# Performance work log

Hardware: AMD Instinct MI355X
Metric: run time of the kernel (lower is better)

## Reference

```python
import jax, jax.numpy as jnp
import numpy as np

KERNEL = 7          # kernel_size
DIL = 1             # dilation
PAD = 3             # padding (same output size for k=7, d=1, s=1)
STRIDE = 1


def setup_inputs() -> dict:
    key = jax.random.key(0)
    x = jax.random.normal(key, (4, 256, 64, 64), dtype=jnp.float32)
    return {"x": x}


def reference(x):
    b, c, h, w = x.shape
    k2 = KERNEL * KERNEL
    # im2col / F.unfold equivalent: (b, c*k2, h_out, w_out), features ordered
    # (channel, kh, kw) exactly like torch.nn.functional.unfold.
    patches = jax.lax.conv_general_dilated_patches(
        x,
        filter_shape=(KERNEL, KERNEL),
        window_strides=(STRIDE, STRIDE),
        padding=[(PAD, PAD), (PAD, PAD)],
        rhs_dilation=(DIL, DIL),
    )
    ho, wo = patches.shape[2], patches.shape[3]
    p = patches.reshape(b, c, k2, ho, wo)          # (b, c, k2, h, w)
    center = p[:, :, k2 // 2]                      # (b, c, h, w) center of window
    # per-pixel similarity of each window element to the center, over channels
    sim = jnp.einsum('bckhw,bchw->bkhw', p, center)  # (b, k2, h, w)
    attn = jax.nn.softmax(sim, axis=1)               # softmax over window dim
    # weighted sum of window features
    out = jnp.einsum('bkhw,bckhw->bchw', attn, p)    # (b, c, h, w)
    return out
```

## Files before the change

### kernel.cpp

```cpp
#include <hip/hip_runtime.h>

typedef float f4 __attribute__((ext_vector_type(4)));

#define Hdim 64
#define Wdim 64
#define Cdim 256
#define HW (Hdim * Wdim)

__global__ __launch_bounds__(512, 4) void selfattn_kernel(const float* __restrict__ x,
                                                          float* __restrict__ out)
{
    const int bid = blockIdx.x;
    const int k   = bid & 7;
    const int seq = bid >> 3;
    const int b   = k >> 1;
    const int h   = (k & 1) * 32 + (seq >> 1);
    const int wbase = (seq & 1) * 32;
    const int t = threadIdx.x;

    __shared__ float simRed[49][32];
    __shared__ float attnBuf[49][32];
    __shared__ float redBuf[7][32];
    __shared__ float psumBuf[7][32];

    const float* xb = x + (size_t)b * (Cdim * HW);

    {
        const int w4 = t & 7;
        const int cp = (t >> 3) & 7;
        const int dy = t >> 6;
        const int lw0 = w4 * 4;
        const int w0g = wbase + lw0;

        if (dy < 7) {
            float sim[7][4];
            #pragma unroll
            for (int dx = 0; dx < 7; ++dx)
                #pragma unroll
                for (int p = 0; p < 4; ++p) sim[dx][p] = 0.f;

            const int row = h + dy - 3;
            if (row >= 0 && row < Hdim) {
                const bool hasL = (w0g != 0);
                const bool hasR = (w0g != 60);
                const float* xr = xb + (size_t)cp * HW + row * Wdim;
                const float* xc = xb + (size_t)cp * HW + h   * Wdim;
                for (int i = 0; i < 32; ++i) {
                    float f[12];
                    if (hasL) {
                        f4 v = *(const f4*)(xr + w0g - 4);
                        f[0]=v.x; f[1]=v.y; f[2]=v.z; f[3]=v.w;
                    } else { f[0]=0.f; f[1]=0.f; f[2]=0.f; f[3]=0.f; }
                    {
                        f4 v = *(const f4*)(xr + w0g);
                        f[4]=v.x; f[5]=v.y; f[6]=v.z; f[7]=v.w;
                    }
                    if (hasR) {
                        f4 v = *(const f4*)(xr + w0g + 4);
                        f[8]=v.x; f[9]=v.y; f[10]=v.z; f[11]=v.w;
                    } else { f[8]=0.f; f[9]=0.f; f[10]=0.f; f[11]=0.f; }
                    f4 cen = *(const f4*)(xc + w0g);
                    #pragma unroll
                    for (int dx = 0; dx < 7; ++dx)
                        #pragma unroll
                        for (int p = 0; p < 4; ++p)
                            sim[dx][p] += cen[p] * f[dx + p + 1];
                    xr += 8 * HW;
                    xc += 8 * HW;
                }
            }
            #pragma unroll
            for (int dx = 0; dx < 7; ++dx)
                #pragma unroll
                for (int p = 0; p < 4; ++p) {
                    float v = sim[dx][p];
                    v += __shfl_xor(v, 8);
                    v += __shfl_xor(v, 16);
                    v += __shfl_xor(v, 32);
                    sim[dx][p] = v;
                }
            if (cp == 0) {
                #pragma unroll
                for (int dx = 0; dx < 7; ++dx)
                    *(f4*)&simRed[dy * 7 + dx][lw0] = *(const f4*)sim[dx];
            }
        }
    }
    __syncthreads();

    {
        const int w  = t & 31;
        const int kc = t >> 5;
        float sred[7], e[7];
        if (kc < 7) {
            float lmax = -3.0e38f;
            #pragma unroll
            for (int jj = 0; jj < 7; ++jj) {
                float s = simRed[kc * 7 + jj][w];
                sred[jj] = s;
                lmax = fmaxf(lmax, s);
            }
            redBuf[kc][w] = lmax;
        }
        __syncthreads();
        if (kc < 7) {
            float m = redBuf[0][w];
            #pragma unroll
            for (int q = 1; q < 7; ++q) m = fmaxf(m, redBuf[q][w]);
            float ps = 0.f;
            #pragma unroll
            for (int jj = 0; jj < 7; ++jj) {
                e[jj] = __expf(sred[jj] - m);
                ps += e[jj];
            }
            psumBuf[kc][w] = ps;
        }
        __syncthreads();
        if (kc < 7) {
            float l = psumBuf[0][w];
            #pragma unroll
            for (int q = 1; q < 7; ++q) l += psumBuf[q][w];
            float rinv = 1.0f / l;
            #pragma unroll
            for (int jj = 0; jj < 7; ++jj)
                attnBuf[kc * 7 + jj][w] = e[jj] * rinv;
        }
    }
    __syncthreads();

    {
        const int w4 = t & 7;
        const int ci = t >> 3;
        const int lw0 = w4 * 4;
        const int w0g = wbase + lw0;
        const int c0 = ci * 4;
        const bool hasL = (w0g != 0);
        const bool hasR = (w0g != 60);

        float acc[4][4];
        #pragma unroll
        for (int ch = 0; ch < 4; ++ch)
            #pragma unroll
            for (int p = 0; p < 4; ++p) acc[ch][p] = 0.f;

        for (int dy = 0; dy < 7; ++dy) {
            const int row = h + dy - 3;
            if (row < 0 || row >= Hdim) continue;
            float a[7][4];
            #pragma unroll
            for (int dx = 0; dx < 7; ++dx) {
                f4 v = *(const f4*)&attnBuf[dy * 7 + dx][lw0];
                a[dx][0]=v.x; a[dx][1]=v.y; a[dx][2]=v.z; a[dx][3]=v.w;
            }
            const float* xr = xb + (size_t)c0 * HW + row * Wdim;
            #pragma unroll
            for (int ch = 0; ch < 4; ++ch) {
                float f[12];
                if (hasL) {
                    f4 v = *(const f4*)(xr + w0g - 4);
                    f[0]=v.x; f[1]=v.y; f[2]=v.z; f[3]=v.w;
                } else { f[0]=0.f; f[1]=0.f; f[2]=0.f; f[3]=0.f; }
                {
                    f4 v = *(const f4*)(xr + w0g);
                    f[4]=v.x; f[5]=v.y; f[6]=v.z; f[7]=v.w;
                }
                if (hasR) {
                    f4 v = *(const f4*)(xr + w0g + 4);
                    f[8]=v.x; f[9]=v.y; f[10]=v.z; f[11]=v.w;
                } else { f[8]=0.f; f[9]=0.f; f[10]=0.f; f[11]=0.f; }
                #pragma unroll
                for (int dx = 0; dx < 7; ++dx)
                    #pragma unroll
                    for (int p = 0; p < 4; ++p)
                        acc[ch][p] += a[dx][p] * f[dx + p + 1];
                xr += HW;
            }
        }

        float* ob = out + (size_t)b * (Cdim * HW) + h * Wdim + wbase;
        #pragma unroll
        for (int ch = 0; ch < 4; ++ch)
            *(f4*)(ob + (size_t)(c0 + ch) * HW + lw0) = *(const f4*)acc[ch];
    }
}

extern "C" void kernel_launch(void* const* d_in, const int* in_sizes, int n_in,
                              void* d_out, int out_size, void* d_ws, size_t ws_size,
                              hipStream_t stream)
{
    const float* x = (const float*)d_in[0];
    float* out = (float*)d_out;
    selfattn_kernel<<<dim3(512), 512, 0, stream>>>(x, out);
}
```

Baseline: 40.31 us.

## Split fused kernel into similarity and output kernels with channel-split grids

Replaces the single fused kernel with two kernels. The first computes partial window similarities over half the channels per block into a workspace. The second sums the two partials, applies the softmax, and computes the weighted output for half the channels per block. Each kernel runs 1024 blocks instead of 512, which raises parallelism and lets the first kernel drop idle threads. The cost is an extra launch, a workspace round trip, and softmax recomputed twice per pixel group. The fused kernel is kept as a fallback when the workspace is too small.

```diff
diff --git a/kernel.cpp b/kernel.cpp
--- a/kernel.cpp
+++ b/kernel.cpp
@@ -7,8 +7,208 @@
 #define Cdim 256
 #define HW (Hdim * Wdim)
 
-__global__ __launch_bounds__(512, 4) void selfattn_kernel(const float* __restrict__ x,
-                                                          float* __restrict__ out)
+
+__global__ __launch_bounds__(448) void k1_sim(const float* __restrict__ x,
+                                              float* __restrict__ ws)
+{
+    const int bid = blockIdx.x;
+    const int k   = bid & 7;
+    const int seq = bid >> 3;
+    const int b   = k >> 1;
+    const int h   = (k & 1) * 32 + (seq >> 2);
+    const int wh  = (seq >> 1) & 1;
+    const int chalf = seq & 1;
+    const int wbase = wh * 32;
+    const int cbase = chalf * 128;
+    const int t = threadIdx.x;
+
+    const int w4 = t & 7;
+    const int cp = (t >> 3) & 7;
+    const int dy = t >> 6;
+    const int lw0 = w4 * 4;
+    const int w0g = wbase + lw0;
+
+    const float* xb = x + (size_t)b * (Cdim * HW);
+
+    float sim[7][4];
+    #pragma unroll
+    for (int dx = 0; dx < 7; ++dx)
+        #pragma unroll
+        for (int p = 0; p < 4; ++p) sim[dx][p] = 0.f;
+
+    const int row = h + dy - 3;
+    if (row >= 0 && row < Hdim) {
+        const bool hasL = (w0g != 0);
+        const bool hasR = (w0g != 60);
+        const float* xr = xb + (size_t)(cbase + cp) * HW + row * Wdim;
+        const float* xc = xb + (size_t)(cbase + cp) * HW + h   * Wdim;
+        #pragma unroll 2
+        for (int i = 0; i < 16; ++i) {
+            float f[12];
+            if (hasL) {
+                f4 v = *(const f4*)(xr + w0g - 4);
+                f[0]=v.x; f[1]=v.y; f[2]=v.z; f[3]=v.w;
+            } else { f[0]=0.f; f[1]=0.f; f[2]=0.f; f[3]=0.f; }
+            {
+                f4 v = *(const f4*)(xr + w0g);
+                f[4]=v.x; f[5]=v.y; f[6]=v.z; f[7]=v.w;
+            }
+            if (hasR) {
+                f4 v = *(const f4*)(xr + w0g + 4);
+                f[8]=v.x; f[9]=v.y; f[10]=v.z; f[11]=v.w;
+            } else { f[8]=0.f; f[9]=0.f; f[10]=0.f; f[11]=0.f; }
+            f4 cen = *(const f4*)(xc + w0g);
+            #pragma unroll
+            for (int dx = 0; dx < 7; ++dx)
+                #pragma unroll
+                for (int p = 0; p < 4; ++p)
+                    sim[dx][p] += cen[p] * f[dx + p + 1];
+            xr += 8 * HW;
+            xc += 8 * HW;
+        }
+    }
+    #pragma unroll
+    for (int dx = 0; dx < 7; ++dx)
+        #pragma unroll
+        for (int p = 0; p < 4; ++p) {
+            float v = sim[dx][p];
+            v += __shfl_xor(v, 8);
+            v += __shfl_xor(v, 16);
+            v += __shfl_xor(v, 32);
+            sim[dx][p] = v;
+        }
+    if (cp == 0) {
+        float* wp = ws + (size_t)bid * (49 * 32);
+        #pragma unroll
+        for (int dx = 0; dx < 7; ++dx)
+            *(f4*)(wp + (dy * 7 + dx) * 32 + lw0) = *(const f4*)sim[dx];
+    }
+}
+
+__global__ __launch_bounds__(512) void k2_out(const float* __restrict__ x,
+                                              const float* __restrict__ ws,
+                                              float* __restrict__ out)
+{
+    const int bid = blockIdx.x;
+    const int k   = bid & 7;
+    const int seq = bid >> 3;
+    const int b   = k >> 1;
+    const int h   = (k & 1) * 32 + (seq >> 2);
+    const int wh  = (seq >> 1) & 1;
+    const int chalf = seq & 1;
+    const int wbase = wh * 32;
+    const int cbase = chalf * 128;
+    const int t = threadIdx.x;
+
+    __shared__ float attnBuf[49][32];
+    __shared__ float redBuf[7][32];
+    __shared__ float psumBuf[7][32];
+
+    const float* xb = x + (size_t)b * (Cdim * HW);
+
+    const int seqBase = ((h & 31) * 4 + wh * 2);
+    const float* p0 = ws + (size_t)((seqBase + 0) * 8 + k) * (49 * 32);
+    const float* p1 = ws + (size_t)((seqBase + 1) * 8 + k) * (49 * 32);
+
+    {
+        const int w  = t & 31;
+        const int kc = t >> 5;
+        float sred[7], e[7];
+        if (kc < 7) {
+            float lmax = -3.0e38f;
+            #pragma unroll
+            for (int jj = 0; jj < 7; ++jj) {
+                const int idx = (kc * 7 + jj) * 32 + w;
+                float s = p0[idx] + p1[idx];
+                sred[jj] = s;
+                lmax = fmaxf(lmax, s);
+            }
+            redBuf[kc][w] = lmax;
+        }
+        __syncthreads();
+        if (kc < 7) {
+            float m = redBuf[0][w];
+            #pragma unroll
+            for (int q = 1; q < 7; ++q) m = fmaxf(m, redBuf[q][w]);
+            float ps = 0.f;
+            #pragma unroll
+            for (int jj = 0; jj < 7; ++jj) {
+                e[jj] = __expf(sred[jj] - m);
+                ps += e[jj];
+            }
+            psumBuf[kc][w] = ps;
+        }
+        __syncthreads();
+        if (kc < 7) {
+            float l = psumBuf[0][w];
+            #pragma unroll
+            for (int q = 1; q < 7; ++q) l += psumBuf[q][w];
+            float rinv = 1.0f / l;
+            #pragma unroll
+            for (int jj = 0; jj < 7; ++jj)
+                attnBuf[kc * 7 + jj][w] = e[jj] * rinv;
+        }
+    }
+    __syncthreads();
+
+    {
+        const int w4 = t & 7;
+        const int ci = t >> 3;
+        const int lw0 = w4 * 4;
+        const int w0g = wbase + lw0;
+        const int c0 = cbase + ci * 2;
+        const bool hasL = (w0g != 0);
+        const bool hasR = (w0g != 60);
+
+        float acc[2][4];
+        #pragma unroll
+        for (int ch = 0; ch < 2; ++ch)
+            #pragma unroll
+            for (int p = 0; p < 4; ++p) acc[ch][p] = 0.f;
+
+        for (int dy = 0; dy < 7; ++dy) {
+            const int row = h + dy - 3;
+            if (row < 0 || row >= Hdim) continue;
+            float a[7][4];
+            #pragma unroll
+            for (int dx = 0; dx < 7; ++dx) {
+                f4 v = *(const f4*)&attnBuf[dy * 7 + dx][lw0];
+                a[dx][0]=v.x; a[dx][1]=v.y; a[dx][2]=v.z; a[dx][3]=v.w;
+            }
+            const float* xr = xb + (size_t)c0 * HW + row * Wdim;
+            #pragma unroll
+            for (int ch = 0; ch < 2; ++ch) {
+                float f[12];
+                if (hasL) {
+                    f4 v = *(const f4*)(xr + w0g - 4);
+                    f[0]=v.x; f[1]=v.y; f[2]=v.z; f[3]=v.w;
+                } else { f[0]=0.f; f[1]=0.f; f[2]=0.f; f[3]=0.f; }
+                {
+                    f4 v = *(const f4*)(xr + w0g);
+                    f[4]=v.x; f[5]=v.y; f[6]=v.z; f[7]=v.w;
+                }
+                if (hasR) {
+                    f4 v = *(const f4*)(xr + w0g + 4);
+                    f[8]=v.x; f[9]=v.y; f[10]=v.z; f[11]=v.w;
+                } else { f[8]=0.f; f[9]=0.f; f[10]=0.f; f[11]=0.f; }
+                #pragma unroll
+                for (int dx = 0; dx < 7; ++dx)
+                    #pragma unroll
+                    for (int p = 0; p < 4; ++p)
+                        acc[ch][p] += a[dx][p] * f[dx + p + 1];
+                xr += HW;
+            }
+        }
+
+        float* ob = out + (size_t)b * (Cdim * HW) + h * Wdim + wbase;
+        #pragma unroll
+        for (int ch = 0; ch < 2; ++ch)
+            *(f4*)(ob + (size_t)(c0 + ch) * HW + lw0) = *(const f4*)acc[ch];
+    }
+}
+
+__global__ __launch_bounds__(512, 4) void selfattn_fallback(const float* __restrict__ x,
+                                                            float* __restrict__ out)
 {
     const int bid = blockIdx.x;
     const int k   = bid & 7;
@@ -190,5 +390,12 @@
 {
     const float* x = (const float*)d_in[0];
     float* out = (float*)d_out;
-    selfattn_kernel<<<dim3(512), 512, 0, stream>>>(x, out);
+    const size_t need = (size_t)1024 * 49 * 32 * 4;
+    if (ws_size >= need) {
+        float* ws = (float*)d_ws;
+        k1_sim<<<dim3(1024), 448, 0, stream>>>(x, ws);
+        k2_out<<<dim3(1024), 512, 0, stream>>>(x, ws, out);
+    } else {
+        selfattn_fallback<<<dim3(512), 512, 0, stream>>>(x, out);
+    }
 }
```

Result: slower. 48.46 us (+20.2%).

## Stage 7-row input tiles in LDS and share them between both passes

Applied to the files above, without the earlier changes.

Both the similarity pass and the weighted-sum pass now work chunk by chunk over 32 channels. For each chunk, 7 input rows covering the full width are copied cooperatively into a 57KB shared-memory buffer, and all threads then read their window values from LDS instead of issuing redundant global loads. The second pass is re-split so threads cover pairs of window rows, with partial sums combined by shuffles before the store, and the two attention buffers are merged into one. The large LDS footprint lowers occupancy (the min-blocks hint is dropped), and the per-chunk barriers add synchronisation. Each block also loads a full 64-wide row even though it only needs 32 columns plus the halo.

```diff
diff --git a/kernel.cpp b/kernel.cpp
--- a/kernel.cpp
+++ b/kernel.cpp
@@ -7,8 +7,8 @@
 #define Cdim 256
 #define HW (Hdim * Wdim)
 
-__global__ __launch_bounds__(512, 4) void selfattn_kernel(const float* __restrict__ x,
-                                                          float* __restrict__ out)
+__global__ __launch_bounds__(512) void selfattn_kernel(const float* __restrict__ x,
+                                                       float* __restrict__ out)
 {
     const int bid = blockIdx.x;
     const int k   = bid & 7;
@@ -18,73 +18,89 @@
     const int wbase = (seq & 1) * 32;
     const int t = threadIdx.x;
 
-    __shared__ float simRed[49][32];
-    __shared__ float attnBuf[49][32];
+    __shared__ __align__(16) float xbuf[32 * 7 * 64];
+    __shared__ __align__(16) float smBuf[49][32];
     __shared__ float redBuf[7][32];
     __shared__ float psumBuf[7][32];
 
     const float* xb = x + (size_t)b * (Cdim * HW);
 
-    {
-        const int w4 = t & 7;
-        const int cp = (t >> 3) & 7;
-        const int dy = t >> 6;
-        const int lw0 = w4 * 4;
-        const int w0g = wbase + lw0;
-
-        if (dy < 7) {
-            float sim[7][4];
-            #pragma unroll
-            for (int dx = 0; dx < 7; ++dx)
-                #pragma unroll
-                for (int p = 0; p < 4; ++p) sim[dx][p] = 0.f;
-
-            const int row = h + dy - 3;
-            if (row >= 0 && row < Hdim) {
-                const bool hasL = (w0g != 0);
-                const bool hasR = (w0g != 60);
-                const float* xr = xb + (size_t)cp * HW + row * Wdim;
-                const float* xc = xb + (size_t)cp * HW + h   * Wdim;
-                for (int i = 0; i < 32; ++i) {
-                    float f[12];
-                    if (hasL) {
-                        f4 v = *(const f4*)(xr + w0g - 4);
-                        f[0]=v.x; f[1]=v.y; f[2]=v.z; f[3]=v.w;
-                    } else { f[0]=0.f; f[1]=0.f; f[2]=0.f; f[3]=0.f; }
-                    {
-                        f4 v = *(const f4*)(xr + w0g);
-                        f[4]=v.x; f[5]=v.y; f[6]=v.z; f[7]=v.w;
-                    }
-                    if (hasR) {
-                        f4 v = *(const f4*)(xr + w0g + 4);
-                        f[8]=v.x; f[9]=v.y; f[10]=v.z; f[11]=v.w;
-                    } else { f[8]=0.f; f[9]=0.f; f[10]=0.f; f[11]=0.f; }
-                    f4 cen = *(const f4*)(xc + w0g);
-                    #pragma unroll
-                    for (int dx = 0; dx < 7; ++dx)
-                        #pragma unroll
-                        for (int p = 0; p < 4; ++p)
-                            sim[dx][p] += cen[p] * f[dx + p + 1];
-                    xr += 8 * HW;
-                    xc += 8 * HW;
-                }
-            }
-            #pragma unroll
-            for (int dx = 0; dx < 7; ++dx)
-                #pragma unroll
-                for (int p = 0; p < 4; ++p) {
-                    float v = sim[dx][p];
-                    v += __shfl_xor(v, 8);
-                    v += __shfl_xor(v, 16);
-                    v += __shfl_xor(v, 32);
-                    sim[dx][p] = v;
-                }
-            if (cp == 0) {
+    int grows[7];
+    #pragma unroll
+    for (int r = 0; r < 7; ++r) {
+        int g = h + r - 3;
+        grows[r] = g < 0 ? 0 : (g > 63 ? 63 : g);
+    }
+    const int scc = t >> 4;
+    const int swq = t & 15;
+
+    const int w4A = t & 7;
+    const int cpA = (t >> 3) & 7;
+    const int dyA = t >> 6;
+    const int lw0A = w4A * 4;
+    const int w0gA = wbase + lw0A;
+    const int rowA = h + dyA - 3;
+    const bool rowAok = (dyA < 7) && (rowA >= 0) && (rowA < Hdim);
+    const bool hasLA = (w0gA != 0);
+    const bool hasRA = (w0gA != 60);
+
+    float sim[7][4];
+    #pragma unroll
+    for (int dx = 0; dx < 7; ++dx)
+        #pragma unroll
+        for (int p = 0; p < 4; ++p) sim[dx][p] = 0.f;
+
+    for (int ch = 0; ch < 8; ++ch) {
+        {
+            const float* sb = xb + (size_t)(ch * 32 + scc) * HW + swq * 4;
+            float* db = &xbuf[(scc * 7) * 64 + swq * 4];
+            #pragma unroll
+            for (int r = 0; r < 7; ++r) {
+                f4 v = *(const f4*)(sb + grows[r] * 64);
+                *(f4*)(db + r * 64) = v;
+            }
+        }
+        __syncthreads();
+        if (rowAok) {
+            #pragma unroll
+            for (int j = 0; j < 4; ++j) {
+                const int cc = cpA + j * 8;
+                const float* rp = &xbuf[(cc * 7 + dyA) * 64];
+                const float* cq = &xbuf[(cc * 7 + 3) * 64];
+                float f[12];
+                if (hasLA) { f4 v = *(const f4*)(rp + w0gA - 4);
+                    f[0]=v.x; f[1]=v.y; f[2]=v.z; f[3]=v.w; }
+                else { f[0]=0.f; f[1]=0.f; f[2]=0.f; f[3]=0.f; }
+                { f4 v = *(const f4*)(rp + w0gA);
+                    f[4]=v.x; f[5]=v.y; f[6]=v.z; f[7]=v.w; }
+                if (hasRA) { f4 v = *(const f4*)(rp + w0gA + 4);
+                    f[8]=v.x; f[9]=v.y; f[10]=v.z; f[11]=v.w; }
+                else { f[8]=0.f; f[9]=0.f; f[10]=0.f; f[11]=0.f; }
+                f4 cen = *(const f4*)(cq + w0gA);
                 #pragma unroll
                 for (int dx = 0; dx < 7; ++dx)
-                    *(f4*)&simRed[dy * 7 + dx][lw0] = *(const f4*)sim[dx];
-            }
-        }
+                    #pragma unroll
+                    for (int p = 0; p < 4; ++p)
+                        sim[dx][p] += cen[p] * f[dx + p + 1];
+            }
+        }
+        __syncthreads();
+    }
+
+    #pragma unroll
+    for (int dx = 0; dx < 7; ++dx)
+        #pragma unroll
+        for (int p = 0; p < 4; ++p) {
+            float v = sim[dx][p];
+            v += __shfl_xor(v, 8);
+            v += __shfl_xor(v, 16);
+            v += __shfl_xor(v, 32);
+            sim[dx][p] = v;
+        }
+    if (dyA < 7 && cpA == 0) {
+        #pragma unroll
+        for (int dx = 0; dx < 7; ++dx)
+            *(f4*)&smBuf[dyA * 7 + dx][lw0A] = *(const f4*)sim[dx];
     }
     __syncthreads();
 
@@ -96,7 +112,7 @@
             float lmax = -3.0e38f;
             #pragma unroll
             for (int jj = 0; jj < 7; ++jj) {
-                float s = simRed[kc * 7 + jj][w];
+                float s = smBuf[kc * 7 + jj][w];
                 sred[jj] = s;
                 lmax = fmaxf(lmax, s);
             }
@@ -123,64 +139,92 @@
             float rinv = 1.0f / l;
             #pragma unroll
             for (int jj = 0; jj < 7; ++jj)
-                attnBuf[kc * 7 + jj][w] = e[jj] * rinv;
+                smBuf[kc * 7 + jj][w] = e[jj] * rinv;
         }
     }
     __syncthreads();
 
-    {
-        const int w4 = t & 7;
-        const int ci = t >> 3;
-        const int lw0 = w4 * 4;
-        const int w0g = wbase + lw0;
-        const int c0 = ci * 4;
-        const bool hasL = (w0g != 0);
-        const bool hasR = (w0g != 60);
-
-        float acc[4][4];
-        #pragma unroll
-        for (int ch = 0; ch < 4; ++ch)
-            #pragma unroll
-            for (int p = 0; p < 4; ++p) acc[ch][p] = 0.f;
-
-        for (int dy = 0; dy < 7; ++dy) {
-            const int row = h + dy - 3;
-            if (row < 0 || row >= Hdim) continue;
-            float a[7][4];
-            #pragma unroll
-            for (int dx = 0; dx < 7; ++dx) {
-                f4 v = *(const f4*)&attnBuf[dy * 7 + dx][lw0];
-                a[dx][0]=v.x; a[dx][1]=v.y; a[dx][2]=v.z; a[dx][3]=v.w;
-            }
-            const float* xr = xb + (size_t)c0 * HW + row * Wdim;
-            #pragma unroll
-            for (int ch = 0; ch < 4; ++ch) {
+    const int w4B = t & 7;
+    const int dup = (t >> 3) & 3;
+    const int ccI = t >> 5;
+    const int lw0B = w4B * 4;
+    const int w0gB = wbase + lw0B;
+    const bool hasLB = (w0gB != 0);
+    const bool hasRB = (w0gB != 60);
+    const int dyB0 = dup * 2;
+    const int dyB1 = dup * 2 + 1;
+    const int rowB0 = h + dyB0 - 3;
+    const int rowB1 = h + dyB1 - 3;
+    const bool ok0 = (rowB0 >= 0) && (rowB0 < Hdim);
+    const bool ok1 = (dyB1 < 7) && (rowB1 >= 0) && (rowB1 < Hdim);
+
+    float a0[7][4], a1[7][4];
+    #pragma unroll
+    for (int dx = 0; dx < 7; ++dx) {
+        f4 v = *(const f4*)&smBuf[dyB0 * 7 + dx][lw0B];
+        a0[dx][0]=v.x; a0[dx][1]=v.y; a0[dx][2]=v.z; a0[dx][3]=v.w;
+        if (dyB1 < 7) {
+            f4 u = *(const f4*)&smBuf[dyB1 * 7 + dx][lw0B];
+            a1[dx][0]=u.x; a1[dx][1]=u.y; a1[dx][2]=u.z; a1[dx][3]=u.w;
+        } else {
+            a1[dx][0]=0.f; a1[dx][1]=0.f; a1[dx][2]=0.f; a1[dx][3]=0.f;
+        }
+    }
+
+    for (int ch = 0; ch < 8; ++ch) {
+        __syncthreads();
+        {
+            const float* sb = xb + (size_t)(ch * 32 + scc) * HW + swq * 4;
+            float* db = &xbuf[(scc * 7) * 64 + swq * 4];
+            #pragma unroll
+            for (int r = 0; r < 7; ++r) {
+                f4 v = *(const f4*)(sb + grows[r] * 64);
+                *(f4*)(db + r * 64) = v;
+            }
+        }
+        __syncthreads();
+
+        float accA[4] = {0.f, 0.f, 0.f, 0.f};
+        float accB[4] = {0.f, 0.f, 0.f, 0.f};
+        #pragma unroll
+        for (int ci = 0; ci < 2; ++ci) {
+            const int cc = ccI + ci * 16;
+            float* acc = ci ? accB : accA;
+            #pragma unroll
+            for (int half = 0; half < 2; ++half) {
+                const int dy = half ? dyB1 : dyB0;
+                const bool ok = half ? ok1 : ok0;
+                if (!ok) continue;
+                const float (*aa)[4] = half ? a1 : a0;
+                const float* rp = &xbuf[(cc * 7 + dy) * 64];
                 float f[12];
-                if (hasL) {
-                    f4 v = *(const f4*)(xr + w0g - 4);
-                    f[0]=v.x; f[1]=v.y; f[2]=v.z; f[3]=v.w;
-                } else { f[0]=0.f; f[1]=0.f; f[2]=0.f; f[3]=0.f; }
-                {
-                    f4 v = *(const f4*)(xr + w0g);
-                    f[4]=v.x; f[5]=v.y; f[6]=v.z; f[7]=v.w;
-                }
-                if (hasR) {
-                    f4 v = *(const f4*)(xr + w0g + 4);
-                    f[8]=v.x; f[9]=v.y; f[10]=v.z; f[11]=v.w;
-                } else { f[8]=0.f; f[9]=0.f; f[10]=0.f; f[11]=0.f; }
+                if (hasLB) { f4 v = *(const f4*)(rp + w0gB - 4);
+                    f[0]=v.x; f[1]=v.y; f[2]=v.z; f[3]=v.w; }
+                else { f[0]=0.f; f[1]=0.f; f[2]=0.f; f[3]=0.f; }
+                { f4 v = *(const f4*)(rp + w0gB);
+                    f[4]=v.x; f[5]=v.y; f[6]=v.z; f[7]=v.w; }
+                if (hasRB) { f4 v = *(const f4*)(rp + w0gB + 4);
+                    f[8]=v.x; f[9]=v.y; f[10]=v.z; f[11]=v.w; }
+                else { f[8]=0.f; f[9]=0.f; f[10]=0.f; f[11]=0.f; }
                 #pragma unroll
                 for (int dx = 0; dx < 7; ++dx)
                     #pragma unroll
                     for (int p = 0; p < 4; ++p)
-                        acc[ch][p] += a[dx][p] * f[dx + p + 1];
-                xr += HW;
-            }
-        }
-
-        float* ob = out + (size_t)b * (Cdim * HW) + h * Wdim + wbase;
-        #pragma unroll
-        for (int ch = 0; ch < 4; ++ch)
-            *(f4*)(ob + (size_t)(c0 + ch) * HW + lw0) = *(const f4*)acc[ch];
+                        acc[p] += aa[dx][p] * f[dx + p + 1];
+            }
+        }
+        #pragma unroll
+        for (int p = 0; p < 4; ++p) {
+            accA[p] += __shfl_xor(accA[p], 8);
+            accA[p] += __shfl_xor(accA[p], 16);
+            accB[p] += __shfl_xor(accB[p], 8);
+            accB[p] += __shfl_xor(accB[p], 16);
+        }
+        if (dup == 0) {
+            float* ob = out + (size_t)b * (Cdim * HW) + h * Wdim + w0gB;
+            *(f4*)(ob + (size_t)(ch * 32 + ccI) * HW)      = *(const f4*)accA;
+            *(f4*)(ob + (size_t)(ch * 32 + ccI + 16) * HW) = *(const f4*)accB;
+        }
     }
 }
 
```

Result: slower. 49.21 us (+22.1%).
